# Performance work log

Measured on AMD Instinct MI355X. Metric: run time of the kernel, lower is better.

The kernel has to match this reference:

```python
import jax, jax.numpy as jnp
import numpy as np

N = 100000
E = 640000
H = 128
C = 16


def setup_inputs() -> dict:
    key = jax.random.key(0)
    ks = jax.random.split(key, 8)
    s = 1.0 / np.sqrt(H)
    return {
        "x": jax.random.normal(ks[0], (N, H), dtype=jnp.float32),
        "edge_index": jax.random.randint(ks[1], (2, E), 0, N, dtype=jnp.int64),
        "W1l": jax.random.uniform(ks[2], (H, H), jnp.float32, -s, s),
        "W1r": jax.random.uniform(ks[3], (H, H), jnp.float32, -s, s),
        "b1": jnp.zeros((H,), jnp.float32),
        "W2l": jax.random.uniform(ks[4], (H, C), jnp.float32, -s, s),
        "W2r": jax.random.uniform(ks[5], (H, C), jnp.float32, -s, s),
        "b2": jnp.zeros((C,), jnp.float32),
    }


def sage_conv(x, src, dst, Wl, Wr, b):
    # mean aggregation of source-node features onto destination nodes
    msg_sum = jax.ops.segment_sum(x[src], dst, num_segments=N)      # [N, d]
    deg = jax.ops.segment_sum(jnp.ones((src.shape[0],), x.dtype), dst, num_segments=N)
    agg = msg_sum / jnp.maximum(deg, 1.0)[:, None]
    # lin_l(agg) + lin_r(x); bias lives in lin_l (PyG SAGEConv default)
    return agg @ Wl + x @ Wr + b


def reference(x, edge_index, W1l, W1r, b1, W2l, W2r, b2):
    src, dst = edge_index[0], edge_index[1]
    h = sage_conv(x, src, dst, W1l, W1r, b1)
    h = jax.nn.relu(h)
    # F.dropout in eval mode == identity (reference run in eval)
    out = sage_conv(h, src, dst, W2l, W2r, b2)
    return out
```

## Files before the change

### kernel.cpp

```cpp
#include <hip/hip_runtime.h>

#define NNODES 100000
#define NEDGES 640000
#define HDIM 128
#define CDIM 16
#define NP 100352
#define SLOTS 32

typedef __attribute__((ext_vector_type(8))) short bf16x8;
typedef __attribute__((ext_vector_type(4))) float f32x4;

union U16x8 { uint4 u; bf16x8 v; };

__device__ __forceinline__ unsigned short f2bf(float f) {
    unsigned int u = __float_as_uint(f);
    unsigned int r = (u + 0x7fffu + ((u >> 16) & 1u)) >> 16;
    return (unsigned short)r;
}
__device__ __forceinline__ float bf2f(unsigned short s) {
    return __uint_as_float(((unsigned int)s) << 16);
}

__global__ __launch_bounds__(256) void binfuse_kernel(
    const int* __restrict__ src, const int* __restrict__ dst,
    int* __restrict__ cnt, int* __restrict__ ebuf,
    const float* __restrict__ x, unsigned short* __restrict__ xb,
    const float* __restrict__ W1l, const float* __restrict__ W1r,
    const float* __restrict__ W2l, const float* __restrict__ W2r,
    unsigned short* __restrict__ w1img, unsigned short* __restrict__ w2img)
{
    const int b = blockIdx.x;
    const int tid = threadIdx.x;
    const int m5 = b % 5;

    int d = 0, s = 0, p = SLOTS;
    if (m5 == 0) {
        int e = (b / 5) * 256 + tid;
        d = dst[e];
        s = src[e];
        p = atomicAdd(&cnt[d], 1);
    }

    {
        int i = b * 256 + tid;
        float4 v = reinterpret_cast<const float4*>(x)[i];
        ushort4 r;
        r.x = f2bf(v.x); r.y = f2bf(v.y); r.z = f2bf(v.z); r.w = f2bf(v.w);
        reinterpret_cast<ushort4*>(xb)[i] = r;
    }

    if (m5 == 0) {
        if (p < SLOTS) ebuf[d * SLOTS + p] = s;
    } else if (m5 == 1 && b < 5 * 144) {
        int idx = (b / 5) * 256 + tid;
        if (idx < 32768) {
            int n = idx >> 8;
            int k = idx & 255;
            float v = (k < 128) ? W1l[k * HDIM + n] : W1r[(k - 128) * HDIM + n];
            int ck = k >> 3;
            w1img[n * 256 + ((ck ^ (n & 7)) << 3) + (k & 7)] = f2bf(v);
        } else {
            int rem = idx - 32768;
            int n = rem >> 7;
            int k = rem & 127;
            float v = (n < 16) ? W2l[k * CDIM + n] : W2r[k * CDIM + (n - 16)];
            int ck = k >> 3;
            w2img[n * 128 + ((ck ^ (n & 7)) << 3) + (k & 7)] = f2bf(v);
        }
    }
}

__global__ __launch_bounds__(256) void gather1_kernel(
    const unsigned short* __restrict__ xb, const int* __restrict__ cnt,
    const int* __restrict__ ebuf, unsigned short* __restrict__ agg)
{
    int t = blockIdx.x * blockDim.x + threadIdx.x;
    int node = t >> 4;
    int c = t & 15;
    if (node >= NNODES) return;
    int deg = cnt[node];
    int n = min(deg, SLOTS);
    const int* eb = ebuf + node * SLOTS;
    float a0 = 0.f, a1 = 0.f, a2 = 0.f, a3 = 0.f, a4 = 0.f, a5 = 0.f, a6 = 0.f, a7 = 0.f;
    int j = 0;
    for (; j + 1 < n; j += 2) {
        int s0 = eb[j], s1 = eb[j + 1];
        uint4 u = reinterpret_cast<const uint4*>(xb)[s0 * 16 + c];
        uint4 v = reinterpret_cast<const uint4*>(xb)[s1 * 16 + c];
        a0 += bf2f(u.x & 0xffff) + bf2f(v.x & 0xffff);
        a1 += bf2f(u.x >> 16)    + bf2f(v.x >> 16);
        a2 += bf2f(u.y & 0xffff) + bf2f(v.y & 0xffff);
        a3 += bf2f(u.y >> 16)    + bf2f(v.y >> 16);
        a4 += bf2f(u.z & 0xffff) + bf2f(v.z & 0xffff);
        a5 += bf2f(u.z >> 16)    + bf2f(v.z >> 16);
        a6 += bf2f(u.w & 0xffff) + bf2f(v.w & 0xffff);
        a7 += bf2f(u.w >> 16)    + bf2f(v.w >> 16);
    }
    if (j < n) {
        int s0 = eb[j];
        uint4 u = reinterpret_cast<const uint4*>(xb)[s0 * 16 + c];
        a0 += bf2f(u.x & 0xffff); a1 += bf2f(u.x >> 16);
        a2 += bf2f(u.y & 0xffff); a3 += bf2f(u.y >> 16);
        a4 += bf2f(u.z & 0xffff); a5 += bf2f(u.z >> 16);
        a6 += bf2f(u.w & 0xffff); a7 += bf2f(u.w >> 16);
    }
    float sc = 1.0f / fmaxf((float)deg, 1.0f);
    uint4 r;
    r.x = (unsigned)f2bf(a0 * sc) | ((unsigned)f2bf(a1 * sc) << 16);
    r.y = (unsigned)f2bf(a2 * sc) | ((unsigned)f2bf(a3 * sc) << 16);
    r.z = (unsigned)f2bf(a4 * sc) | ((unsigned)f2bf(a5 * sc) << 16);
    r.w = (unsigned)f2bf(a6 * sc) | ((unsigned)f2bf(a7 * sc) << 16);
    reinterpret_cast<uint4*>(agg)[node * 16 + c] = r;
}

__global__ __launch_bounds__(256) void gather2_kernel(
    const float* __restrict__ pq, const int* __restrict__ cnt,
    const int* __restrict__ ebuf, float* __restrict__ out)
{
    int t = blockIdx.x * blockDim.x + threadIdx.x;
    int node = t >> 2;
    int c = t & 3;
    if (node >= NNODES) return;
    int deg = cnt[node];
    int n = min(deg, SLOTS);
    const int* eb = ebuf + node * SLOTS;
    float ax = 0.f, ay = 0.f, az = 0.f, aw = 0.f;
    int j = 0;
    for (; j + 1 < n; j += 2) {
        int s0 = eb[j], s1 = eb[j + 1];
        float4 v0 = reinterpret_cast<const float4*>(pq)[s0 * 8 + c];
        float4 v1 = reinterpret_cast<const float4*>(pq)[s1 * 8 + c];
        ax += v0.x + v1.x; ay += v0.y + v1.y; az += v0.z + v1.z; aw += v0.w + v1.w;
    }
    if (j < n) {
        int s0 = eb[j];
        float4 v0 = reinterpret_cast<const float4*>(pq)[s0 * 8 + c];
        ax += v0.x; ay += v0.y; az += v0.z; aw += v0.w;
    }
    float sc = 1.0f / fmaxf((float)deg, 1.0f);
    float4 q = reinterpret_cast<const float4*>(pq)[node * 8 + 4 + c];
    float4 r;
    r.x = ax * sc + q.x; r.y = ay * sc + q.y; r.z = az * sc + q.z; r.w = aw * sc + q.w;
    reinterpret_cast<float4*>(out)[node * 4 + c] = r;
}

__global__ __launch_bounds__(512, 2) void gemm_fused_kernel(
    const unsigned short* __restrict__ agg, const unsigned short* __restrict__ xb,
    const unsigned short* __restrict__ w1img, const unsigned short* __restrict__ w2img,
    const float* __restrict__ b1, const float* __restrict__ b2,
    float* __restrict__ pq)
{
    __shared__ alignas(16) unsigned short Wt[128 * 256];

    const int tid = threadIdx.x;
    {
        const uint4* wsrc = reinterpret_cast<const uint4*>(w1img);
        uint4* wdst = reinterpret_cast<uint4*>(Wt);
        #pragma unroll
        for (int j = 0; j < 8; ++j) wdst[tid + j * 512] = wsrc[tid + j * 512];
    }
    __syncthreads();

    const int wave = tid >> 6;
    const int lane = tid & 63;
    const int lm = lane & 15;
    const int lq = lane >> 4;

    float bv[8];
    #pragma unroll
    for (int ct = 0; ct < 8; ++ct) bv[ct] = b1[ct * 16 + lm];
    const float bq = b2[lm];

    const uint4* aggv = reinterpret_cast<const uint4*>(agg);
    const uint4* xbv  = reinterpret_cast<const uint4*>(xb);

    const int row0 = blockIdx.x * 128;

    {
        int row = row0 + wave * 16 + lm;
        bool valid = row < NNODES;
        size_t abase = (size_t)row * 16 + lq;

        U16x8 af[8];
        uint4 z = make_uint4(0u, 0u, 0u, 0u);
        #pragma unroll
        for (int kt = 0; kt < 4; ++kt) af[kt].u = valid ? aggv[abase + kt * 4] : z;
        #pragma unroll
        for (int kt = 0; kt < 4; ++kt) af[4 + kt].u = valid ? xbv[abase + kt * 4] : z;

        f32x4 acc[8];
        #pragma unroll
        for (int c = 0; c < 8; ++c) acc[c] = (f32x4)(0.0f);

        #pragma unroll
        for (int kt = 0; kt < 8; ++kt) {
            int c = kt * 4 + lq;
            #pragma unroll
            for (int ct = 0; ct < 8; ++ct) {
                int n = ct * 16 + lm;
                bf16x8 b = *reinterpret_cast<const bf16x8*>(&Wt[n * 256 + ((c ^ (n & 7)) << 3)]);
                acc[ct] = __builtin_amdgcn_mfma_f32_16x16x32_bf16(af[kt].v, b, acc[ct], 0, 0, 0);
            }
        }

        __syncthreads();

        #pragma unroll
        for (int i = 0; i < 4; ++i) {
            int r = wave * 16 + lq * 4 + i;
            #pragma unroll
            for (int ct = 0; ct < 8; ++ct) {
                float v = fmaxf(acc[ct][i] + bv[ct], 0.0f);
                Wt[r * 136 + ct * 16 + lm] = f2bf(v);
            }
        }
    }
    {
        uint4 w = reinterpret_cast<const uint4*>(w2img)[tid];
        reinterpret_cast<uint4*>(&Wt[17408])[tid] = w;
    }
    __syncthreads();

    {
        const unsigned short* W2 = &Wt[17408];
        const int arow = wave * 16 + lm;

        U16x8 a2[4];
        #pragma unroll
        for (int kt = 0; kt < 4; ++kt)
            a2[kt].v = *reinterpret_cast<const bf16x8*>(&Wt[arow * 136 + kt * 32 + lq * 8]);

        f32x4 acc2[2];
        acc2[0] = (f32x4)(0.0f);
        acc2[1] = (f32x4)(0.0f);

        #pragma unroll
        for (int kt = 0; kt < 4; ++kt) {
            int c = kt * 4 + lq;
            #pragma unroll
            for (int ct = 0; ct < 2; ++ct) {
                int n = ct * 16 + lm;
                bf16x8 b = *reinterpret_cast<const bf16x8*>(&W2[n * 128 + ((c ^ (n & 7)) << 3)]);
                acc2[ct] = __builtin_amdgcn_mfma_f32_16x16x32_bf16(a2[kt].v, b, acc2[ct], 0, 0, 0);
            }
        }

        #pragma unroll
        for (int ct = 0; ct < 2; ++ct) {
            int col = ct * 16 + lm;
            float bvv = (ct == 1) ? bq : 0.0f;
            #pragma unroll
            for (int i = 0; i < 4; ++i) {
                int r = row0 + wave * 16 + lq * 4 + i;
                if (r < NNODES)
                    pq[(size_t)r * 32 + col] = acc2[ct][i] + bvv;
            }
        }
    }
}

extern "C" void kernel_launch(void* const* d_in, const int* in_sizes, int n_in,
                              void* d_out, int out_size, void* d_ws, size_t ws_size,
                              hipStream_t stream) {
    const float* x   = (const float*)d_in[0];
    const int*   ei  = (const int*)d_in[1];
    const float* W1l = (const float*)d_in[2];
    const float* W1r = (const float*)d_in[3];
    const float* b1  = (const float*)d_in[4];
    const float* W2l = (const float*)d_in[5];
    const float* W2r = (const float*)d_in[6];
    const float* b2  = (const float*)d_in[7];
    float* out = (float*)d_out;

    const int* src = ei;
    const int* dst = ei + NEDGES;

    int* cnt  = (int*)d_ws;
    int* ebuf = cnt + NP;
    unsigned short* xb  = (unsigned short*)(ebuf + (size_t)NNODES * SLOTS);
    unsigned short* agg = xb + (size_t)NNODES * HDIM;
    float* pq = (float*)(agg + (size_t)NNODES * HDIM);
    unsigned short* w1img = (unsigned short*)(pq + (size_t)NNODES * 32);
    unsigned short* w2img = w1img + 32768;

    hipMemsetAsync(cnt, 0, NP * sizeof(int), stream);

    binfuse_kernel<<<12500, 256, 0, stream>>>(src, dst, cnt, ebuf, x, xb,
                                              W1l, W1r, W2l, W2r, w1img, w2img);

    gather1_kernel<<<(NNODES * 16 + 255) / 256, 256, 0, stream>>>(xb, cnt, ebuf, agg);

    int ntiles1 = (NNODES + 127) / 128;
    gemm_fused_kernel<<<ntiles1, 512, 0, stream>>>(agg, xb, w1img, w2img, b1, b2, pq);

    gather2_kernel<<<(NNODES * 4 + 255) / 256, 256, 0, stream>>>(pq, cnt, ebuf, out);
}
```

Measured before the change: 189.9 us.

## Fuse layer-1 neighbor gather into the fused GEMM kernel

Result: no change. 189.0 us (-0.5%).

```diff
diff --git a/kernel.cpp b/kernel.cpp
--- a/kernel.cpp
+++ b/kernel.cpp
@@ -19,6 +19,13 @@
 }
 __device__ __forceinline__ float bf2f(unsigned short s) {
     return __uint_as_float(((unsigned int)s) << 16);
+}
+
+__device__ __forceinline__ void acc8(float (&a)[8], uint4 u) {
+    a[0] += bf2f(u.x & 0xffff); a[1] += bf2f(u.x >> 16);
+    a[2] += bf2f(u.y & 0xffff); a[3] += bf2f(u.y >> 16);
+    a[4] += bf2f(u.z & 0xffff); a[5] += bf2f(u.z >> 16);
+    a[6] += bf2f(u.w & 0xffff); a[7] += bf2f(u.w >> 16);
 }
 
 __global__ __launch_bounds__(256) void binfuse_kernel(
@@ -56,9 +63,11 @@
         if (idx < 32768) {
             int n = idx >> 8;
             int k = idx & 255;
-            float v = (k < 128) ? W1l[k * HDIM + n] : W1r[(k - 128) * HDIM + n];
-            int ck = k >> 3;
-            w1img[n * 256 + ((ck ^ (n & 7)) << 3) + (k & 7)] = f2bf(v);
+            int half = k >> 7;
+            int kk = k & 127;
+            float v = half ? W1r[kk * HDIM + n] : W1l[kk * HDIM + n];
+            int ck = kk >> 3;
+            w1img[half * 16384 + n * 128 + ((ck ^ (n & 7)) << 3) + (kk & 7)] = f2bf(v);
         } else {
             int rem = idx - 32768;
             int n = rem >> 7;
@@ -70,47 +79,177 @@
     }
 }
 
-__global__ __launch_bounds__(256) void gather1_kernel(
+__global__ __launch_bounds__(512, 4) void gemm_fused_kernel(
     const unsigned short* __restrict__ xb, const int* __restrict__ cnt,
-    const int* __restrict__ ebuf, unsigned short* __restrict__ agg)
+    const int* __restrict__ ebuf,
+    const unsigned short* __restrict__ w1img, const unsigned short* __restrict__ w2img,
+    const float* __restrict__ b1, const float* __restrict__ b2,
+    float* __restrict__ pq)
 {
-    int t = blockIdx.x * blockDim.x + threadIdx.x;
-    int node = t >> 4;
-    int c = t & 15;
-    if (node >= NNODES) return;
-    int deg = cnt[node];
-    int n = min(deg, SLOTS);
-    const int* eb = ebuf + node * SLOTS;
-    float a0 = 0.f, a1 = 0.f, a2 = 0.f, a3 = 0.f, a4 = 0.f, a5 = 0.f, a6 = 0.f, a7 = 0.f;
-    int j = 0;
-    for (; j + 1 < n; j += 2) {
-        int s0 = eb[j], s1 = eb[j + 1];
-        uint4 u = reinterpret_cast<const uint4*>(xb)[s0 * 16 + c];
-        uint4 v = reinterpret_cast<const uint4*>(xb)[s1 * 16 + c];
-        a0 += bf2f(u.x & 0xffff) + bf2f(v.x & 0xffff);
-        a1 += bf2f(u.x >> 16)    + bf2f(v.x >> 16);
-        a2 += bf2f(u.y & 0xffff) + bf2f(v.y & 0xffff);
-        a3 += bf2f(u.y >> 16)    + bf2f(v.y >> 16);
-        a4 += bf2f(u.z & 0xffff) + bf2f(v.z & 0xffff);
-        a5 += bf2f(u.z >> 16)    + bf2f(v.z >> 16);
-        a6 += bf2f(u.w & 0xffff) + bf2f(v.w & 0xffff);
-        a7 += bf2f(u.w >> 16)    + bf2f(v.w >> 16);
-    }
-    if (j < n) {
-        int s0 = eb[j];
-        uint4 u = reinterpret_cast<const uint4*>(xb)[s0 * 16 + c];
-        a0 += bf2f(u.x & 0xffff); a1 += bf2f(u.x >> 16);
-        a2 += bf2f(u.y & 0xffff); a3 += bf2f(u.y >> 16);
-        a4 += bf2f(u.z & 0xffff); a5 += bf2f(u.z >> 16);
-        a6 += bf2f(u.w & 0xffff); a7 += bf2f(u.w >> 16);
-    }
-    float sc = 1.0f / fmaxf((float)deg, 1.0f);
-    uint4 r;
-    r.x = (unsigned)f2bf(a0 * sc) | ((unsigned)f2bf(a1 * sc) << 16);
-    r.y = (unsigned)f2bf(a2 * sc) | ((unsigned)f2bf(a3 * sc) << 16);
-    r.z = (unsigned)f2bf(a4 * sc) | ((unsigned)f2bf(a5 * sc) << 16);
-    r.w = (unsigned)f2bf(a6 * sc) | ((unsigned)f2bf(a7 * sc) << 16);
-    reinterpret_cast<uint4*>(agg)[node * 16 + c] = r;
+    __shared__ alignas(16) unsigned short LW[128 * 128];
+    __shared__ alignas(16) unsigned short Hs[128 * 136];
+
+    const int tid = threadIdx.x;
+    const int wave = tid >> 6;
+    const int lane = tid & 63;
+    const int lm = lane & 15;
+    const int lq = lane >> 4;
+    const int row0 = blockIdx.x * 128;
+    const int row = row0 + wave * 16 + lm;
+    const bool valid = row < NNODES;
+
+    {
+        const uint4* wsrc = reinterpret_cast<const uint4*>(w1img);
+        uint4* wdst = reinterpret_cast<uint4*>(LW);
+        #pragma unroll
+        for (int j = 0; j < 4; ++j) wdst[tid + j * 512] = wsrc[tid + j * 512];
+    }
+
+    const uint4* xbv = reinterpret_cast<const uint4*>(xb);
+
+    float ag[4][8];
+    #pragma unroll
+    for (int kt = 0; kt < 4; ++kt) {
+        #pragma unroll
+        for (int i = 0; i < 8; ++i) ag[kt][i] = 0.0f;
+    }
+    int deg = 0;
+    if (valid) {
+        deg = cnt[row];
+        int n = min(deg, SLOTS);
+        const int* eb = ebuf + row * SLOTS;
+        int j = 0;
+        for (; j + 1 < n; j += 2) {
+            int s0 = eb[j], s1 = eb[j + 1];
+            size_t b0 = (size_t)s0 * 16 + lq;
+            size_t b1v = (size_t)s1 * 16 + lq;
+            #pragma unroll
+            for (int kt = 0; kt < 4; ++kt) {
+                uint4 u = xbv[b0 + kt * 4];
+                uint4 v = xbv[b1v + kt * 4];
+                acc8(ag[kt], u);
+                acc8(ag[kt], v);
+            }
+        }
+        if (j < n) {
+            int s0 = eb[j];
+            size_t b0 = (size_t)s0 * 16 + lq;
+            #pragma unroll
+            for (int kt = 0; kt < 4; ++kt) acc8(ag[kt], xbv[b0 + kt * 4]);
+        }
+    }
+    const float sc = 1.0f / fmaxf((float)deg, 1.0f);
+
+    U16x8 af[8];
+    #pragma unroll
+    for (int kt = 0; kt < 4; ++kt) {
+        uint4 r;
+        r.x = (unsigned)f2bf(ag[kt][0] * sc) | ((unsigned)f2bf(ag[kt][1] * sc) << 16);
+        r.y = (unsigned)f2bf(ag[kt][2] * sc) | ((unsigned)f2bf(ag[kt][3] * sc) << 16);
+        r.z = (unsigned)f2bf(ag[kt][4] * sc) | ((unsigned)f2bf(ag[kt][5] * sc) << 16);
+        r.w = (unsigned)f2bf(ag[kt][6] * sc) | ((unsigned)f2bf(ag[kt][7] * sc) << 16);
+        af[kt].u = r;
+    }
+    {
+        uint4 z = make_uint4(0u, 0u, 0u, 0u);
+        size_t abase = (size_t)row * 16 + lq;
+        #pragma unroll
+        for (int kt = 0; kt < 4; ++kt) af[4 + kt].u = valid ? xbv[abase + kt * 4] : z;
+    }
+
+    float bv[8];
+    #pragma unroll
+    for (int ct = 0; ct < 8; ++ct) bv[ct] = b1[ct * 16 + lm];
+    const float bq = b2[lm];
+
+    f32x4 acc[8];
+    #pragma unroll
+    for (int c = 0; c < 8; ++c) acc[c] = (f32x4)(0.0f);
+
+    __syncthreads();
+
+    #pragma unroll
+    for (int kt = 0; kt < 4; ++kt) {
+        int c = kt * 4 + lq;
+        #pragma unroll
+        for (int ct = 0; ct < 8; ++ct) {
+            int n = ct * 16 + lm;
+            bf16x8 bfrag = *reinterpret_cast<const bf16x8*>(&LW[n * 128 + ((c ^ (n & 7)) << 3)]);
+            acc[ct] = __builtin_amdgcn_mfma_f32_16x16x32_bf16(af[kt].v, bfrag, acc[ct], 0, 0, 0);
+        }
+    }
+    __syncthreads();
+
+    {
+        const uint4* wsrc = reinterpret_cast<const uint4*>(w1img + 16384);
+        uint4* wdst = reinterpret_cast<uint4*>(LW);
+        #pragma unroll
+        for (int j = 0; j < 4; ++j) wdst[tid + j * 512] = wsrc[tid + j * 512];
+    }
+    __syncthreads();
+
+    #pragma unroll
+    for (int kt = 0; kt < 4; ++kt) {
+        int c = kt * 4 + lq;
+        #pragma unroll
+        for (int ct = 0; ct < 8; ++ct) {
+            int n = ct * 16 + lm;
+            bf16x8 bfrag = *reinterpret_cast<const bf16x8*>(&LW[n * 128 + ((c ^ (n & 7)) << 3)]);
+            acc[ct] = __builtin_amdgcn_mfma_f32_16x16x32_bf16(af[4 + kt].v, bfrag, acc[ct], 0, 0, 0);
+        }
+    }
+    __syncthreads();
+
+    {
+        uint4 w = reinterpret_cast<const uint4*>(w2img)[tid];
+        reinterpret_cast<uint4*>(LW)[tid] = w;
+    }
+    #pragma unroll
+    for (int i = 0; i < 4; ++i) {
+        int r = wave * 16 + lq * 4 + i;
+        #pragma unroll
+        for (int ct = 0; ct < 8; ++ct) {
+            float v = fmaxf(acc[ct][i] + bv[ct], 0.0f);
+            Hs[r * 136 + ct * 16 + lm] = f2bf(v);
+        }
+    }
+    __syncthreads();
+
+    {
+        const int arow = wave * 16 + lm;
+
+        U16x8 a2[4];
+        #pragma unroll
+        for (int kt = 0; kt < 4; ++kt)
+            a2[kt].v = *reinterpret_cast<const bf16x8*>(&Hs[arow * 136 + kt * 32 + lq * 8]);
+
+        f32x4 acc2[2];
+        acc2[0] = (f32x4)(0.0f);
+        acc2[1] = (f32x4)(0.0f);
+
+        #pragma unroll
+        for (int kt = 0; kt < 4; ++kt) {
+            int c = kt * 4 + lq;
+            #pragma unroll
+            for (int ct = 0; ct < 2; ++ct) {
+                int n = ct * 16 + lm;
+                bf16x8 bfrag = *reinterpret_cast<const bf16x8*>(&LW[n * 128 + ((c ^ (n & 7)) << 3)]);
+                acc2[ct] = __builtin_amdgcn_mfma_f32_16x16x32_bf16(a2[kt].v, bfrag, acc2[ct], 0, 0, 0);
+            }
+        }
+
+        #pragma unroll
+        for (int ct = 0; ct < 2; ++ct) {
+            int col = ct * 16 + lm;
+            float bvv = (ct == 1) ? bq : 0.0f;
+            #pragma unroll
+            for (int i = 0; i < 4; ++i) {
+                int r = row0 + wave * 16 + lq * 4 + i;
+                if (r < NNODES)
+                    pq[(size_t)r * 32 + col] = acc2[ct][i] + bvv;
+            }
+        }
+    }
 }
 
 __global__ __launch_bounds__(256) void gather2_kernel(
@@ -144,121 +283,6 @@
     reinterpret_cast<float4*>(out)[node * 4 + c] = r;
 }
 
-__global__ __launch_bounds__(512, 2) void gemm_fused_kernel(
-    const unsigned short* __restrict__ agg, const unsigned short* __restrict__ xb,
-    const unsigned short* __restrict__ w1img, const unsigned short* __restrict__ w2img,
-    const float* __restrict__ b1, const float* __restrict__ b2,
-    float* __restrict__ pq)
-{
-    __shared__ alignas(16) unsigned short Wt[128 * 256];
-
-    const int tid = threadIdx.x;
-    {
-        const uint4* wsrc = reinterpret_cast<const uint4*>(w1img);
-        uint4* wdst = reinterpret_cast<uint4*>(Wt);
-        #pragma unroll
-        for (int j = 0; j < 8; ++j) wdst[tid + j * 512] = wsrc[tid + j * 512];
-    }
-    __syncthreads();
-
-    const int wave = tid >> 6;
-    const int lane = tid & 63;
-    const int lm = lane & 15;
-    const int lq = lane >> 4;
-
-    float bv[8];
-    #pragma unroll
-    for (int ct = 0; ct < 8; ++ct) bv[ct] = b1[ct * 16 + lm];
-    const float bq = b2[lm];
-
-    const uint4* aggv = reinterpret_cast<const uint4*>(agg);
-    const uint4* xbv  = reinterpret_cast<const uint4*>(xb);
-
-    const int row0 = blockIdx.x * 128;
-
-    {
-        int row = row0 + wave * 16 + lm;
-        bool valid = row < NNODES;
-        size_t abase = (size_t)row * 16 + lq;
-
-        U16x8 af[8];
-        uint4 z = make_uint4(0u, 0u, 0u, 0u);
-        #pragma unroll
-        for (int kt = 0; kt < 4; ++kt) af[kt].u = valid ? aggv[abase + kt * 4] : z;
-        #pragma unroll
-        for (int kt = 0; kt < 4; ++kt) af[4 + kt].u = valid ? xbv[abase + kt * 4] : z;
-
-        f32x4 acc[8];
-        #pragma unroll
-        for (int c = 0; c < 8; ++c) acc[c] = (f32x4)(0.0f);
-
-        #pragma unroll
-        for (int kt = 0; kt < 8; ++kt) {
-            int c = kt * 4 + lq;
-            #pragma unroll
-            for (int ct = 0; ct < 8; ++ct) {
-                int n = ct * 16 + lm;
-                bf16x8 b = *reinterpret_cast<const bf16x8*>(&Wt[n * 256 + ((c ^ (n & 7)) << 3)]);
-                acc[ct] = __builtin_amdgcn_mfma_f32_16x16x32_bf16(af[kt].v, b, acc[ct], 0, 0, 0);
-            }
-        }
-
-        __syncthreads();
-
-        #pragma unroll
-        for (int i = 0; i < 4; ++i) {
-            int r = wave * 16 + lq * 4 + i;
-            #pragma unroll
-            for (int ct = 0; ct < 8; ++ct) {
-                float v = fmaxf(acc[ct][i] + bv[ct], 0.0f);
-                Wt[r * 136 + ct * 16 + lm] = f2bf(v);
-            }
-        }
-    }
-    {
-        uint4 w = reinterpret_cast<const uint4*>(w2img)[tid];
-        reinterpret_cast<uint4*>(&Wt[17408])[tid] = w;
-    }
-    __syncthreads();
-
-    {
-        const unsigned short* W2 = &Wt[17408];
-        const int arow = wave * 16 + lm;
-
-        U16x8 a2[4];
-        #pragma unroll
-        for (int kt = 0; kt < 4; ++kt)
-            a2[kt].v = *reinterpret_cast<const bf16x8*>(&Wt[arow * 136 + kt * 32 + lq * 8]);
-
-        f32x4 acc2[2];
-        acc2[0] = (f32x4)(0.0f);
-        acc2[1] = (f32x4)(0.0f);
-
-        #pragma unroll
-        for (int kt = 0; kt < 4; ++kt) {
-            int c = kt * 4 + lq;
-            #pragma unroll
-            for (int ct = 0; ct < 2; ++ct) {
-                int n = ct * 16 + lm;
-                bf16x8 b = *reinterpret_cast<const bf16x8*>(&W2[n * 128 + ((c ^ (n & 7)) << 3)]);
-                acc2[ct] = __builtin_amdgcn_mfma_f32_16x16x32_bf16(a2[kt].v, b, acc2[ct], 0, 0, 0);
-            }
-        }
-
-        #pragma unroll
-        for (int ct = 0; ct < 2; ++ct) {
-            int col = ct * 16 + lm;
-            float bvv = (ct == 1) ? bq : 0.0f;
-            #pragma unroll
-            for (int i = 0; i < 4; ++i) {
-                int r = row0 + wave * 16 + lq * 4 + i;
-                if (r < NNODES)
-                    pq[(size_t)r * 32 + col] = acc2[ct][i] + bvv;
-            }
-        }
-    }
-}
-
 extern "C" void kernel_launch(void* const* d_in, const int* in_sizes, int n_in,
                               void* d_out, int out_size, void* d_ws, size_t ws_size,
                               hipStream_t stream) {
@@ -278,8 +302,7 @@
     int* cnt  = (int*)d_ws;
     int* ebuf = cnt + NP;
     unsigned short* xb  = (unsigned short*)(ebuf + (size_t)NNODES * SLOTS);
-    unsigned short* agg = xb + (size_t)NNODES * HDIM;
-    float* pq = (float*)(agg + (size_t)NNODES * HDIM);
+    float* pq = (float*)(xb + (size_t)NNODES * HDIM);
     unsigned short* w1img = (unsigned short*)(pq + (size_t)NNODES * 32);
     unsigned short* w2img = w1img + 32768;
 
@@ -288,10 +311,8 @@
     binfuse_kernel<<<12500, 256, 0, stream>>>(src, dst, cnt, ebuf, x, xb,
                                               W1l, W1r, W2l, W2r, w1img, w2img);
 
-    gather1_kernel<<<(NNODES * 16 + 255) / 256, 256, 0, stream>>>(xb, cnt, ebuf, agg);
-
     int ntiles1 = (NNODES + 127) / 128;
-    gemm_fused_kernel<<<ntiles1, 512, 0, stream>>>(agg, xb, w1img, w2img, b1, b2, pq);
+    gemm_fused_kernel<<<ntiles1, 512, 0, stream>>>(xb, cnt, ebuf, w1img, w2img, b1, b2, pq);
 
     gather2_kernel<<<(NNODES * 4 + 255) / 256, 256, 0, stream>>>(pq, cnt, ebuf, out);
 }
```
